# Kernel tuning notes

Measured on AMD Instinct MI355X. Metric: run time of the kernel, lower is better.

## Reference

```python
import math
import jax, jax.numpy as jnp
import numpy as np
from jax import lax

B, H, W = 8, 96, 96
FC, R, P, KS, TOPK = 768, 12, 16, 13, 24
SUP_TH, SUP_MIX, OPEN_K, DIL, NMS = 0.28, 0.8, 3, 3, 3

# prototype anchor metadata (buffers, deterministic)
ORI = jnp.asarray(np.linspace(0.0, math.pi, P + 1)[:-1], jnp.float32)
_lenL = np.array([0.4, 0.7, 1.0, 1.25], np.float32)
_widL = np.array([0.12, 0.18, 0.24, 0.3], np.float32)
LEN = jnp.asarray(_lenL[np.arange(P) % 4])
WID = jnp.asarray(_widL[(np.arange(P) // 4) % 4])
_ax = np.linspace(-1.0, 1.0, KS).astype(np.float32)
_gy, _gx = np.meshgrid(_ax, _ax, indexing='ij')
GX, GY = jnp.asarray(_gx), jnp.asarray(_gy)


def conv2d(x, w, b, pad=0):
    y = lax.conv_general_dilated(x, w, (1, 1), [(pad, pad), (pad, pad)],
                                 dimension_numbers=('NCHW', 'OIHW', 'NCHW'))
    return y + b[None, :, None, None]


def maxpool(x, k):
    p = k // 2
    return lax.reduce_window(x, -jnp.inf, lax.max, (1, 1, k, k), (1, 1, 1, 1),
                             [(0, 0), (0, 0), (p, p), (p, p)])


def avgpool3(x):
    s = lax.reduce_window(x, 0.0, lax.add, (1, 1, 3, 3), (1, 1, 1, 1),
                          [(0, 0), (0, 0), (1, 1), (1, 1)])
    return s / 9.0  # torch count_include_pad=True


def normalize_map(t):
    mn = t.min(axis=(-2, -1), keepdims=True)
    mx = t.max(axis=(-2, -1), keepdims=True)
    return (t - mn) / jnp.maximum(mx - mn, 1e-6)


def binary_open(m, k):
    er = 1.0 - maxpool(1.0 - m, k)
    return jnp.clip(maxpool(er, k), 0.0, 1.0)


def support_mask_fn(carrier_hp, density):
    cs = normalize_map(avgpool3(jnp.abs(carrier_hp)))
    ds = normalize_map(density)
    ev = SUP_MIX * cs + (1.0 - SUP_MIX) * ds
    m = (ev >= SUP_TH).astype(carrier_hp.dtype)
    m = binary_open(m, OPEN_K)
    m = maxpool(m, DIL)
    return jnp.clip(m, 0.0, 1.0)


def setup_inputs() -> dict:
    key = jax.random.key(0)
    ks = jax.random.split(key, 16)
    d = {
        'features': jax.random.normal(ks[0], (B, FC, H, W), jnp.float32),
        'carrier_hp': jax.random.normal(ks[1], (B, 1, H, W), jnp.float32),
        'density': jax.random.uniform(ks[2], (B, 1, H, W), jnp.float32),
        # feature_project: 1x1 conv FC->R, 3x3 conv R->R
        'w1': jax.random.normal(ks[3], (R, FC, 1, 1), jnp.float32) * (1.0 / math.sqrt(FC)),
        'b1': jnp.zeros((R,), jnp.float32),
        'w2': jax.random.normal(ks[4], (R, R, 3, 3), jnp.float32) * (1.0 / math.sqrt(R * 9)),
        'b2': jnp.zeros((R,), jnp.float32),
        # post_mix: 1x1 conv (R+4)->R, 1x1 conv R->FC
        'w3': jax.random.normal(ks[5], (R, R + 4, 1, 1), jnp.float32) * (1.0 / math.sqrt(R + 4)),
        'b3': jnp.zeros((R,), jnp.float32),
        'w4': jax.random.normal(ks[6], (FC, R, 1, 1), jnp.float32) * (1.0 / math.sqrt(R)),
        'b4': jnp.zeros((FC,), jnp.float32),
        'proto': jax.random.normal(ks[7], (P, R), jnp.float32) * 0.02,
    }
    return d


def reference(features, carrier_hp, density, w1, b1, w2, b2, w3, b3, w4, b4, proto):
    gelu = lambda x: jax.nn.gelu(x, approximate=False)
    # 1) feature projection
    proj = gelu(conv2d(gelu(conv2d(features, w1, b1, 0)), w2, b2, 1))  # [B,R,H,W]
    # 2) occupancy + support
    occ = normalize_map(jnp.abs(proj).mean(axis=1, keepdims=True))      # [B,1,H,W]
    sup = support_mask_fn(carrier_hp, density)                          # [B,1,H,W]
    # 3) NMS + top-k anchors
    scores = occ * sup
    local_max = maxpool(scores, NMS)
    peak = ((scores >= local_max) & (scores > 0.05)).astype(scores.dtype)
    flat = (scores * peak).reshape(B, -1)
    vals, idx = lax.top_k(flat, TOPK)                                   # [B,K]
    anchor_map = jnp.zeros_like(flat).at[jnp.arange(B)[:, None], idx].set(vals)
    anchor_map = anchor_map.reshape(B, 1, H, W)
    ys, xs = idx // W, idx % W
    # 4) per-anchor prototype selection
    proj_flat = proj.reshape(B, R, H * W)
    feat_at = jnp.take_along_axis(proj_flat, jnp.broadcast_to(idx[:, None, :], (B, R, TOPK)), axis=2)  # [B,R,K]
    logits = jnp.einsum('brk,pr->bkp', feat_at, proto)
    pidx = jnp.argmax(logits, axis=-1)                                  # [B,K]
    ori, ln, wd = ORI[pidx], LEN[pidx], WID[pidx]
    # 5) oriented Gaussian footprints [B,K,KS,KS]
    c = jnp.cos(ori)[..., None, None]
    s = jnp.sin(ori)[..., None, None]
    xr = c * GX + s * GY
    yr = -s * GX + c * GY
    foot = jnp.exp(-(xr / ln[..., None, None]) ** 2 - (yr / wd[..., None, None]) ** 2)
    foot = foot * vals[..., None, None]
    emb = proto[pidx]                                                   # [B,K,R]
    contrib = emb[:, :, :, None, None] * foot[:, :, None]               # [B,K,R,KS,KS]
    # 6) scatter-stamp onto canvas
    off = jnp.arange(KS) - KS // 2
    yy = ys[:, :, None, None] + off[None, None, :, None]                # [B,K,KS,KS]
    xx = xs[:, :, None, None] + off[None, None, None, :]
    valid = ((yy >= 0) & (yy < H) & (xx >= 0) & (xx < W)).astype(contrib.dtype)
    yyc = jnp.clip(yy, 0, H - 1)
    xxc = jnp.clip(xx, 0, W - 1)

    def stamp(ctr, y2, x2, v):
        c0 = jnp.zeros((R, H, W), ctr.dtype)
        return c0.at[:, y2, x2].add(jnp.transpose(ctr, (1, 0, 2, 3)) * v[None])

    canvas = jax.vmap(stamp)(contrib, yyc, xxc, valid)                  # [B,R,H,W]
    # 7) support-lock + post mix
    canvas = canvas * sup
    extras = jnp.concatenate([occ, sup, anchor_map, normalize_map(density)], axis=1)
    mixed = conv2d(gelu(conv2d(jnp.concatenate([canvas, extras], axis=1), w3, b3, 0)), w4, b4, 0)
    return mixed
```

## Files before the change

kernel.cpp:

```cpp
#include <hip/hip_runtime.h>
#include <math.h>

#define Bn 8
#define Hh 96
#define Ww 96
#define NPIX 9216
#define FCn 768
#define Rr 12
#define Pp 16
#define KSn 13
#define TOPKn 24
#define CAPc 1536
#define NSPLIT 8

__device__ __forceinline__ float gelu_f(float x) {
  return 0.5f * x * (1.0f + erff(x * 0.70710678118654752440f));
}

__global__ __launch_bounds__(256) void k_conv1_part(
    const float* __restrict__ feat, const float* __restrict__ w1,
    float* __restrict__ partial) {
  __shared__ float w1s[96 * 12];
  int s = blockIdx.x & 7;
  int pixblk = blockIdx.x >> 3;
  int c0 = s * 96;
  for (int i = threadIdx.x; i < 96 * 12; i += 256) {
    int c = i / 12, r = i % 12;
    w1s[i] = w1[r * FCn + c0 + c];
  }
  __syncthreads();
  int px0 = pixblk * 512 + threadIdx.x * 2;
  int b = px0 / NPIX, hw = px0 % NPIX;
  const float* fb = feat + (size_t)b * FCn * NPIX + (size_t)c0 * NPIX + hw;
  float acc0[12], acc1[12];
#pragma unroll
  for (int r = 0; r < 12; r++) { acc0[r] = 0.f; acc1[r] = 0.f; }
  for (int c = 0; c < 96; c += 4) {
    float2 f[4];
#pragma unroll
    for (int u = 0; u < 4; u++)
      f[u] = *(const float2*)(fb + (size_t)(c + u) * NPIX);
#pragma unroll
    for (int u = 0; u < 4; u++) {
#pragma unroll
      for (int r = 0; r < 12; r++) {
        float w = w1s[(c + u) * 12 + r];
        acc0[r] = fmaf(f[u].x, w, acc0[r]);
        acc1[r] = fmaf(f[u].y, w, acc1[r]);
      }
    }
  }
  float* outp = partial + (size_t)s * (Bn * Rr * NPIX) +
                (size_t)b * Rr * NPIX + hw;
#pragma unroll
  for (int r = 0; r < 12; r++)
    *(float2*)(outp + (size_t)r * NPIX) = make_float2(acc0[r], acc1[r]);
}

__global__ __launch_bounds__(256) void k_bias_gelu(
    const float* __restrict__ partial, const float* __restrict__ b1,
    float* __restrict__ t1, unsigned int* __restrict__ statsu) {
  int e4 = blockIdx.x * 256 + threadIdx.x;
  const int Q = (Bn * Rr * NPIX) / 4;
  const float4* pp = (const float4*)partial;
  float4 v = pp[e4];
#pragma unroll
  for (int s = 1; s < NSPLIT; s++) {
    float4 t = pp[e4 + s * Q];
    v.x += t.x; v.y += t.y; v.z += t.z; v.w += t.w;
  }
  int r = (e4 / (NPIX / 4)) % Rr;
  float bias = b1[r];
  float4 o;
  o.x = gelu_f(v.x + bias);
  o.y = gelu_f(v.y + bias);
  o.z = gelu_f(v.z + bias);
  o.w = gelu_f(v.w + bias);
  ((float4*)t1)[e4] = o;
  if (e4 < 24) {
    statsu[e4 * 2 + 0] = 0x7f800000u;
    statsu[e4 * 2 + 1] = 0u;
  }
}

__global__ __launch_bounds__(256) void k_conv2(
    const float* __restrict__ t1, const float* __restrict__ w2,
    const float* __restrict__ b2, const float* __restrict__ carrier,
    const float* __restrict__ density, float* __restrict__ proj,
    float* __restrict__ occ_raw, float* __restrict__ cs_raw,
    unsigned int* __restrict__ statsu, float* __restrict__ canvas,
    float* __restrict__ anchor) {
  __shared__ float w2s[Rr * Rr * 9];
  __shared__ float b2s[Rr];
  for (int i = threadIdx.x; i < Rr * Rr * 9; i += 256) w2s[i] = w2[i];
  if (threadIdx.x < Rr) b2s[threadIdx.x] = b2[threadIdx.x];
  int pix = blockIdx.x * 256 + threadIdx.x;
  {
    float4 z = make_float4(0.f, 0.f, 0.f, 0.f);
    float4* c4 = (float4*)canvas;
#pragma unroll
    for (int q = 0; q < 3; q++) c4[(size_t)q * (Bn * NPIX) + pix] = z;
    anchor[pix] = 0.f;
  }
  __syncthreads();
  int b = pix / NPIX, hw = pix % NPIX;
  int y = hw / Ww, x = hw % Ww;
  float acc[12];
#pragma unroll
  for (int r = 0; r < 12; r++) acc[r] = 0.f;
  const float* tb = t1 + (size_t)b * Rr * NPIX;
  for (int ri = 0; ri < Rr; ri++) {
    const float* tc = tb + (size_t)ri * NPIX;
#pragma unroll
    for (int ky = 0; ky < 3; ky++) {
      int yy = y + ky - 1;
      if (yy < 0 || yy >= Hh) continue;
#pragma unroll
      for (int kx = 0; kx < 3; kx++) {
        int xx = x + kx - 1;
        if (xx < 0 || xx >= Ww) continue;
        float v = tc[yy * Ww + xx];
#pragma unroll
        for (int ro = 0; ro < 12; ro++)
          acc[ro] = fmaf(v, w2s[((ro * Rr + ri) * 3 + ky) * 3 + kx], acc[ro]);
      }
    }
  }
  float asum = 0.f;
  float* pb = proj + (size_t)b * Rr * NPIX + hw;
#pragma unroll
  for (int ro = 0; ro < 12; ro++) {
    float g = gelu_f(acc[ro] + b2s[ro]);
    pb[(size_t)ro * NPIX] = g;
    asum += fabsf(g);
  }
  float occv = asum / 12.0f;
  occ_raw[pix] = occv;

  const float* cb = carrier + (size_t)b * NPIX;
  float s9 = 0.f;
  for (int dy = -1; dy <= 1; dy++) {
    int yy = y + dy;
    if (yy < 0 || yy >= Hh) continue;
    for (int dx = -1; dx <= 1; dx++) {
      int xx = x + dx;
      if (xx < 0 || xx >= Ww) continue;
      s9 += fabsf(cb[yy * Ww + xx]);
    }
  }
  float csv = s9 / 9.0f;
  cs_raw[pix] = csv;
  float dv = density[pix];

  float mn0 = occv, mx0 = occv, mn1 = csv, mx1 = csv, mn2 = dv, mx2 = dv;
#pragma unroll
  for (int off = 32; off > 0; off >>= 1) {
    mn0 = fminf(mn0, __shfl_xor(mn0, off));
    mx0 = fmaxf(mx0, __shfl_xor(mx0, off));
    mn1 = fminf(mn1, __shfl_xor(mn1, off));
    mx1 = fmaxf(mx1, __shfl_xor(mx1, off));
    mn2 = fminf(mn2, __shfl_xor(mn2, off));
    mx2 = fmaxf(mx2, __shfl_xor(mx2, off));
  }
  if ((threadIdx.x & 63) == 0) {
    atomicMin(&statsu[(0 * Bn + b) * 2 + 0], __float_as_uint(mn0));
    atomicMax(&statsu[(0 * Bn + b) * 2 + 1], __float_as_uint(mx0));
    atomicMin(&statsu[(1 * Bn + b) * 2 + 0], __float_as_uint(mn1));
    atomicMax(&statsu[(1 * Bn + b) * 2 + 1], __float_as_uint(mx1));
    atomicMin(&statsu[(2 * Bn + b) * 2 + 0], __float_as_uint(mn2));
    atomicMax(&statsu[(2 * Bn + b) * 2 + 1], __float_as_uint(mx2));
  }
}

__global__ __launch_bounds__(1024) void k_support_topk(
    const float* __restrict__ occ_raw, const float* __restrict__ cs_raw,
    const float* __restrict__ density, const float* __restrict__ stats,
    float* __restrict__ occ, float* __restrict__ ds, float* __restrict__ sup,
    float* __restrict__ vals, int* __restrict__ idxs,
    float* __restrict__ anchor) {
  __shared__ unsigned char mA[NPIX], mB[NPIX];
  __shared__ float flat[NPIX];
  __shared__ float cval[CAPc];
  __shared__ int cidx[CAPc];
  __shared__ int cnt;
  __shared__ float rv[16];
  __shared__ int ri[16], rs[16];
  int b = blockIdx.x;
  const int tid = threadIdx.x;
  const int lane = tid & 63, wid = tid >> 6;
  float omn = stats[(0 * Bn + b) * 2], omx = stats[(0 * Bn + b) * 2 + 1];
  float cmn = stats[(1 * Bn + b) * 2], cmx = stats[(1 * Bn + b) * 2 + 1];
  float dmn = stats[(2 * Bn + b) * 2], dmx = stats[(2 * Bn + b) * 2 + 1];
  float oiv = fmaxf(omx - omn, 1e-6f);
  float civ = fmaxf(cmx - cmn, 1e-6f);
  float div_ = fmaxf(dmx - dmn, 1e-6f);
  if (tid == 0) cnt = 0;
  float occ9[9];
#pragma unroll
  for (int i = 0; i < 9; i++) {
    int p = tid + i * 1024;
    float oc = (occ_raw[b * NPIX + p] - omn) / oiv;
    float cv = (cs_raw[b * NPIX + p] - cmn) / civ;
    float dv = (density[b * NPIX + p] - dmn) / div_;
    occ[b * NPIX + p] = oc;
    ds[b * NPIX + p] = dv;
    occ9[i] = oc;
    float ev = 0.8f * cv + 0.2f * dv;
    mA[p] = (ev >= 0.28f) ? 1 : 0;
  }
  __syncthreads();
#pragma unroll
  for (int i = 0; i < 9; i++) {
    int p = tid + i * 1024;
    int y = p / Ww, x = p % Ww;
    unsigned char m = 1;
    for (int dy = -1; dy <= 1; dy++) {
      int yy = y + dy;
      if (yy < 0 || yy >= Hh) continue;
      for (int dx = -1; dx <= 1; dx++) {
        int xx = x + dx;
        if (xx < 0 || xx >= Ww) continue;
        m = (unsigned char)(m & mA[yy * Ww + xx]);
      }
    }
    mB[p] = m;
  }
  __syncthreads();
#pragma unroll
  for (int i = 0; i < 9; i++) {
    int p = tid + i * 1024;
    int y = p / Ww, x = p % Ww;
    unsigned char m = 0;
    for (int dy = -1; dy <= 1; dy++) {
      int yy = y + dy;
      if (yy < 0 || yy >= Hh) continue;
      for (int dx = -1; dx <= 1; dx++) {
        int xx = x + dx;
        if (xx < 0 || xx >= Ww) continue;
        m = (unsigned char)(m | mB[yy * Ww + xx]);
      }
    }
    mA[p] = m;
  }
  __syncthreads();
#pragma unroll
  for (int i = 0; i < 9; i++) {
    int p = tid + i * 1024;
    int y = p / Ww, x = p % Ww;
    unsigned char m = 0;
    for (int dy = -1; dy <= 1; dy++) {
      int yy = y + dy;
      if (yy < 0 || yy >= Hh) continue;
      for (int dx = -1; dx <= 1; dx++) {
        int xx = x + dx;
        if (xx < 0 || xx >= Ww) continue;
        m = (unsigned char)(m | mA[yy * Ww + xx]);
      }
    }
    float sv = (float)m;
    sup[b * NPIX + p] = sv;
    flat[p] = occ9[i] * sv;
  }
  __syncthreads();
  float pk[9];
#pragma unroll
  for (int i = 0; i < 9; i++) {
    int p = tid + i * 1024;
    int y = p / Ww, x = p % Ww;
    float s = flat[p];
    float lm = -INFINITY;
    for (int dy = -1; dy <= 1; dy++) {
      int yy = y + dy;
      if (yy < 0 || yy >= Hh) continue;
      for (int dx = -1; dx <= 1; dx++) {
        int xx = x + dx;
        if (xx < 0 || xx >= Ww) continue;
        lm = fmaxf(lm, flat[yy * Ww + xx]);
      }
    }
    pk[i] = (s >= lm && s > 0.05f) ? s : 0.0f;
  }
  __syncthreads();
#pragma unroll
  for (int i = 0; i < 9; i++) {
    int p = tid + i * 1024;
    flat[p] = pk[i];
    if (pk[i] > 0.f) {
      int slot = atomicAdd(&cnt, 1);
      if (slot < CAPc) {
        cval[slot] = pk[i];
        cidx[slot] = p;
      }
    }
  }
  __syncthreads();
  const int C = cnt;
  if (C <= CAPc) {
    for (int k = 0; k < TOPKn; k++) {
      float bv = -INFINITY;
      int bi = 0x7fffffff, bs = -1;
      for (int j = tid; j < C; j += 1024) {
        float v = cval[j];
        int pi = cidx[j];
        if (v > bv || (v == bv && pi < bi)) {
          bv = v;
          bi = pi;
          bs = j;
        }
      }
      for (int off = 32; off > 0; off >>= 1) {
        float ov = __shfl_xor(bv, off);
        int oi = __shfl_xor(bi, off);
        int os = __shfl_xor(bs, off);
        if (ov > bv || (ov == bv && oi < bi)) {
          bv = ov;
          bi = oi;
          bs = os;
        }
      }
      if (lane == 0) {
        rv[wid] = bv;
        ri[wid] = bi;
        rs[wid] = bs;
      }
      __syncthreads();
      if (tid == 0) {
        float Bv = rv[0];
        int Bi = ri[0], Bs = rs[0];
        for (int w = 1; w < 16; w++) {
          if (rv[w] > Bv || (rv[w] == Bv && ri[w] < Bi)) {
            Bv = rv[w];
            Bi = ri[w];
            Bs = rs[w];
          }
        }
        if (Bv > 0.f) {
          vals[b * TOPKn + k] = Bv;
          idxs[b * TOPKn + k] = Bi;
          anchor[b * NPIX + Bi] = Bv;
          cval[Bs] = -INFINITY;
        } else {
          vals[b * TOPKn + k] = 0.f;
          idxs[b * TOPKn + k] = 0;
        }
      }
      __syncthreads();
    }
  } else {
    for (int k = 0; k < TOPKn; k++) {
      float bv = -INFINITY;
      int bi = 0x7fffffff;
      for (int p = tid; p < NPIX; p += 1024) {
        float v = flat[p];
        if (v > bv || (v == bv && p < bi)) {
          bv = v;
          bi = p;
        }
      }
      for (int off = 32; off > 0; off >>= 1) {
        float ov = __shfl_xor(bv, off);
        int oi = __shfl_xor(bi, off);
        if (ov > bv || (ov == bv && oi < bi)) {
          bv = ov;
          bi = oi;
        }
      }
      if (lane == 0) {
        rv[wid] = bv;
        ri[wid] = bi;
      }
      __syncthreads();
      if (tid == 0) {
        float Bv = rv[0];
        int Bi = ri[0];
        for (int w = 1; w < 16; w++) {
          if (rv[w] > Bv || (rv[w] == Bv && ri[w] < Bi)) {
            Bv = rv[w];
            Bi = ri[w];
          }
        }
        if (Bv > 0.f) {
          vals[b * TOPKn + k] = Bv;
          idxs[b * TOPKn + k] = Bi;
          anchor[b * NPIX + Bi] = Bv;
          flat[Bi] = -INFINITY;
        } else {
          vals[b * TOPKn + k] = 0.f;
          idxs[b * TOPKn + k] = 0;
        }
      }
      __syncthreads();
    }
  }
}

__global__ __launch_bounds__(192) void k_stamp(
    const float* __restrict__ proj, const float* __restrict__ proto,
    const float* __restrict__ vals, const int* __restrict__ idxs,
    float* __restrict__ canvas) {
  int b = blockIdx.x / TOPKn, k = blockIdx.x % TOPKn;
  __shared__ float embs[12];
  __shared__ float prm[5];
  __shared__ int ppos[2];
  if (threadIdx.x == 0) {
    int id = idxs[b * TOPKn + k];
    float v = vals[b * TOPKn + k];
    float ft[12];
    for (int r = 0; r < 12; r++)
      ft[r] = proj[(size_t)(b * Rr + r) * NPIX + id];
    float bestL = -INFINITY;
    int bp = 0;
    for (int p = 0; p < Pp; p++) {
      float L = 0.f;
      for (int r = 0; r < 12; r++) L = fmaf(ft[r], proto[p * Rr + r], L);
      if (L > bestL) {
        bestL = L;
        bp = p;
      }
    }
    const float lenL[4] = {0.4f, 0.7f, 1.0f, 1.25f};
    const float widL[4] = {0.12f, 0.18f, 0.24f, 0.3f};
    float ori = (float)((M_PI / 16.0) * (double)bp);
    prm[0] = cosf(ori);
    prm[1] = sinf(ori);
    prm[2] = lenL[bp & 3];
    prm[3] = widL[(bp >> 2) & 3];
    prm[4] = v;
    ppos[0] = id / Ww;
    ppos[1] = id % Ww;
    for (int r = 0; r < 12; r++) embs[r] = proto[bp * Rr + r];
  }
  __syncthreads();
  float v = prm[4];
  if (v <= 0.f) return;
  int t = threadIdx.x;
  if (t >= KSn * KSn) return;
  int i = t / KSn, j = t % KSn;
  float gx = (float)(-1.0 + (double)j * (1.0 / 6.0));
  float gy = (float)(-1.0 + (double)i * (1.0 / 6.0));
  float c = prm[0], s = prm[1];
  float xr = c * gx + s * gy;
  float yr = -s * gx + c * gy;
  float tx = xr / prm[2], ty = yr / prm[3];
  float foot = expf(-(tx * tx) - (ty * ty)) * v;
  int yy = ppos[0] + i - KSn / 2;
  int xx = ppos[1] + j - KSn / 2;
  if (yy < 0 || yy >= Hh || xx < 0 || xx >= Ww) return;
  float* cp = canvas + (size_t)b * Rr * NPIX + yy * Ww + xx;
#pragma unroll
  for (int r = 0; r < 12; r++) atomicAdd(cp + (size_t)r * NPIX, embs[r] * foot);
}

__global__ __launch_bounds__(256) void k_post1(
    const float* __restrict__ canvas, const float* __restrict__ sup,
    const float* __restrict__ occ, const float* __restrict__ anchor,
    const float* __restrict__ ds, const float* __restrict__ w3,
    const float* __restrict__ b3, float* __restrict__ h) {
  __shared__ float w3s[12 * 16], b3s[12];
  for (int i = threadIdx.x; i < 192; i += 256) w3s[i] = w3[i];
  if (threadIdx.x < 12) b3s[threadIdx.x] = b3[threadIdx.x];
  __syncthreads();
  int pix = blockIdx.x * 256 + threadIdx.x;
  int b = pix / NPIX, hw = pix % NPIX;
  float in16[16];
  float sv = sup[pix];
#pragma unroll
  for (int r = 0; r < 12; r++)
    in16[r] = canvas[(size_t)(b * Rr + r) * NPIX + hw] * sv;
  in16[12] = occ[pix];
  in16[13] = sv;
  in16[14] = anchor[pix];
  in16[15] = ds[pix];
  float* hb = h + (size_t)b * Rr * NPIX + hw;
#pragma unroll
  for (int ro = 0; ro < 12; ro++) {
    float acc = 0.f;
#pragma unroll
    for (int ci = 0; ci < 16; ci++)
      acc = fmaf(in16[ci], w3s[ro * 16 + ci], acc);
    hb[(size_t)ro * NPIX] = gelu_f(acc + b3s[ro]);
  }
}

__global__ __launch_bounds__(256) void k_post2(
    const float* __restrict__ h, const float* __restrict__ w4,
    const float* __restrict__ b4, float* __restrict__ out) {
  __shared__ float w4s[16 * 12], b4s[16];
  int bx = blockIdx.x;
  int hwblk = bx % 9;
  int g = (bx / 9) % 48;
  int b = bx / (9 * 48);
  int oc0 = g * 16;
  for (int i = threadIdx.x; i < 192; i += 256) w4s[i] = w4[oc0 * 12 + i];
  if (threadIdx.x < 16) b4s[threadIdx.x] = b4[oc0 + threadIdx.x];
  __syncthreads();
  int hw = hwblk * 1024 + threadIdx.x * 4;
  const float* hb = h + (size_t)b * Rr * NPIX + hw;
  float4 hreg[12];
#pragma unroll
  for (int r = 0; r < 12; r++)
    hreg[r] = *(const float4*)(hb + (size_t)r * NPIX);
  float* ob = out + (size_t)(b * FCn + oc0) * NPIX + hw;
#pragma unroll
  for (int j = 0; j < 16; j++) {
    float ax = 0.f, ay = 0.f, az = 0.f, aw = 0.f;
#pragma unroll
    for (int r = 0; r < 12; r++) {
      float w = w4s[j * 12 + r];
      ax = fmaf(hreg[r].x, w, ax);
      ay = fmaf(hreg[r].y, w, ay);
      az = fmaf(hreg[r].z, w, az);
      aw = fmaf(hreg[r].w, w, aw);
    }
    float bb = b4s[j];
    *(float4*)(ob + (size_t)j * NPIX) =
        make_float4(ax + bb, ay + bb, az + bb, aw + bb);
  }
}

extern "C" void kernel_launch(void* const* d_in, const int* in_sizes, int n_in,
                              void* d_out, int out_size, void* d_ws,
                              size_t ws_size, hipStream_t stream) {
  const float* features = (const float*)d_in[0];
  const float* carrier = (const float*)d_in[1];
  const float* density = (const float*)d_in[2];
  const float* w1 = (const float*)d_in[3];
  const float* b1 = (const float*)d_in[4];
  const float* w2 = (const float*)d_in[5];
  const float* b2 = (const float*)d_in[6];
  const float* w3 = (const float*)d_in[7];
  const float* b3 = (const float*)d_in[8];
  const float* w4 = (const float*)d_in[9];
  const float* b4 = (const float*)d_in[10];
  const float* proto = (const float*)d_in[11];
  float* out = (float*)d_out;
  float* ws = (float*)d_ws;

  const size_t NT = (size_t)Bn * Rr * NPIX;
  float* t1 = ws;
  float* partial = ws + NT;
  float* proj = partial;
  float* canvas = partial + NT;
  float* h = partial + 2 * NT;
  float* sm = ws + 9 * NT;
  float* occ_raw = sm;
  float* cs_raw = sm + (size_t)Bn * NPIX;
  float* occ = sm + 2 * (size_t)Bn * NPIX;
  float* ds = sm + 3 * (size_t)Bn * NPIX;
  float* sup = sm + 4 * (size_t)Bn * NPIX;
  float* anchor = sm + 5 * (size_t)Bn * NPIX;
  float* stats = sm + 6 * (size_t)Bn * NPIX;
  unsigned int* statsu = (unsigned int*)stats;
  float* vals = stats + 64;
  int* idxs = (int*)(vals + Bn * TOPKn);

  k_conv1_part<<<144 * NSPLIT, 256, 0, stream>>>(features, w1, partial);
  k_bias_gelu<<<(int)(NT / 4 / 256), 256, 0, stream>>>(partial, b1, t1, statsu);
  k_conv2<<<288, 256, 0, stream>>>(t1, w2, b2, carrier, density, proj, occ_raw,
                                   cs_raw, statsu, canvas, anchor);
  k_support_topk<<<Bn, 1024, 0, stream>>>(occ_raw, cs_raw, density, stats, occ,
                                          ds, sup, vals, idxs, anchor);
  k_stamp<<<Bn * TOPKn, 192, 0, stream>>>(proj, proto, vals, idxs, canvas);
  k_post1<<<288, 256, 0, stream>>>(canvas, sup, occ, anchor, ds, w3, b3, h);
  k_post2<<<Bn * 48 * 9, 256, 0, stream>>>(h, w4, b4, out);
}
```

Before: 577.6 us.

## Fold support-mask computation into conv1 launch and halve channel split

The support-mask pipeline (carrier avgpool, density normalization, morphological open and dilate) moves out of the serial 8-block topk kernel into 8 extra blocks of the conv1 launch, so it runs alongside the bandwidth-bound 1x1 conv. Each of those blocks computes its own carrier and density min/max with an intra-block reduction, so the cross-block atomics for those statistics are dropped. The conv1 channel split goes from 8 to 4, which halves the partial-sum traffic read by bias_gelu but gives each block twice as many channels and fewer blocks overall. The support blocks recompute the 3x3 carrier sums twice, and each is a single 256-thread block that may finish after the conv blocks, lengthening that launch.

```diff
diff --git a/kernel.cpp b/kernel.cpp
--- a/kernel.cpp
+++ b/kernel.cpp
@@ -11,50 +11,173 @@
 #define KSn 13
 #define TOPKn 24
 #define CAPc 1536
-#define NSPLIT 8
+#define NSPLIT 4
 
 __device__ __forceinline__ float gelu_f(float x) {
   return 0.5f * x * (1.0f + erff(x * 0.70710678118654752440f));
 }
 
-__global__ __launch_bounds__(256) void k_conv1_part(
+__global__ __launch_bounds__(256) void k_conv1_sup(
     const float* __restrict__ feat, const float* __restrict__ w1,
-    float* __restrict__ partial) {
-  __shared__ float w1s[96 * 12];
-  int s = blockIdx.x & 7;
-  int pixblk = blockIdx.x >> 3;
-  int c0 = s * 96;
-  for (int i = threadIdx.x; i < 96 * 12; i += 256) {
-    int c = i / 12, r = i % 12;
-    w1s[i] = w1[r * FCn + c0 + c];
-  }
-  __syncthreads();
-  int px0 = pixblk * 512 + threadIdx.x * 2;
-  int b = px0 / NPIX, hw = px0 % NPIX;
-  const float* fb = feat + (size_t)b * FCn * NPIX + (size_t)c0 * NPIX + hw;
-  float acc0[12], acc1[12];
-#pragma unroll
-  for (int r = 0; r < 12; r++) { acc0[r] = 0.f; acc1[r] = 0.f; }
-  for (int c = 0; c < 96; c += 4) {
-    float2 f[4];
-#pragma unroll
-    for (int u = 0; u < 4; u++)
-      f[u] = *(const float2*)(fb + (size_t)(c + u) * NPIX);
-#pragma unroll
-    for (int u = 0; u < 4; u++) {
-#pragma unroll
-      for (int r = 0; r < 12; r++) {
-        float w = w1s[(c + u) * 12 + r];
-        acc0[r] = fmaf(f[u].x, w, acc0[r]);
-        acc1[r] = fmaf(f[u].y, w, acc1[r]);
-      }
-    }
-  }
-  float* outp = partial + (size_t)s * (Bn * Rr * NPIX) +
-                (size_t)b * Rr * NPIX + hw;
-#pragma unroll
-  for (int r = 0; r < 12; r++)
-    *(float2*)(outp + (size_t)r * NPIX) = make_float2(acc0[r], acc1[r]);
+    float* __restrict__ partial, const float* __restrict__ carrier,
+    const float* __restrict__ density, float* __restrict__ sup,
+    float* __restrict__ ds) {
+  __shared__ __align__(16) unsigned char lds_raw[2 * NPIX];
+  __shared__ float red[16];
+  const int tid = threadIdx.x;
+  if (blockIdx.x >= 8) {
+    float* w1s = (float*)lds_raw;
+    int bx = blockIdx.x - 8;
+    int s = bx & 3;
+    int pixblk = bx >> 2;
+    int c0 = s * 192;
+    for (int i = tid; i < 192 * 12; i += 256) {
+      int c = i / 12, r = i % 12;
+      w1s[i] = w1[r * FCn + c0 + c];
+    }
+    __syncthreads();
+    int px0 = pixblk * 512 + tid * 2;
+    int b = px0 / NPIX, hw = px0 % NPIX;
+    const float* fb = feat + (size_t)b * FCn * NPIX + (size_t)c0 * NPIX + hw;
+    float acc0[12], acc1[12];
+#pragma unroll
+    for (int r = 0; r < 12; r++) { acc0[r] = 0.f; acc1[r] = 0.f; }
+    for (int c = 0; c < 192; c += 4) {
+      float2 f[4];
+#pragma unroll
+      for (int u = 0; u < 4; u++)
+        f[u] = *(const float2*)(fb + (size_t)(c + u) * NPIX);
+#pragma unroll
+      for (int u = 0; u < 4; u++) {
+#pragma unroll
+        for (int r = 0; r < 12; r++) {
+          float w = w1s[(c + u) * 12 + r];
+          acc0[r] = fmaf(f[u].x, w, acc0[r]);
+          acc1[r] = fmaf(f[u].y, w, acc1[r]);
+        }
+      }
+    }
+    float* outp = partial + (size_t)s * (Bn * Rr * NPIX) +
+                  (size_t)b * Rr * NPIX + hw;
+#pragma unroll
+    for (int r = 0; r < 12; r++)
+      *(float2*)(outp + (size_t)r * NPIX) = make_float2(acc0[r], acc1[r]);
+    return;
+  }
+  unsigned char* mA = lds_raw;
+  unsigned char* mB = lds_raw + NPIX;
+  int b = blockIdx.x;
+  const int lane = tid & 63, wid = tid >> 6;
+  const float* cb = carrier + (size_t)b * NPIX;
+  const float* db = density + (size_t)b * NPIX;
+  float cmn = INFINITY, cmx = -INFINITY, dmn = INFINITY, dmx = -INFINITY;
+  for (int i = 0; i < 36; i++) {
+    int p = tid + (i << 8);
+    int y = p / Ww, x = p % Ww;
+    float s9 = 0.f;
+    for (int dy = -1; dy <= 1; dy++) {
+      int yy = y + dy;
+      if (yy < 0 || yy >= Hh) continue;
+      for (int dx = -1; dx <= 1; dx++) {
+        int xx = x + dx;
+        if (xx < 0 || xx >= Ww) continue;
+        s9 += fabsf(cb[yy * Ww + xx]);
+      }
+    }
+    float cs = s9 / 9.0f;
+    cmn = fminf(cmn, cs);
+    cmx = fmaxf(cmx, cs);
+    float dv = db[p];
+    dmn = fminf(dmn, dv);
+    dmx = fmaxf(dmx, dv);
+  }
+#pragma unroll
+  for (int off = 32; off > 0; off >>= 1) {
+    cmn = fminf(cmn, __shfl_xor(cmn, off));
+    cmx = fmaxf(cmx, __shfl_xor(cmx, off));
+    dmn = fminf(dmn, __shfl_xor(dmn, off));
+    dmx = fmaxf(dmx, __shfl_xor(dmx, off));
+  }
+  if (lane == 0) {
+    red[wid * 4 + 0] = cmn;
+    red[wid * 4 + 1] = cmx;
+    red[wid * 4 + 2] = dmn;
+    red[wid * 4 + 3] = dmx;
+  }
+  __syncthreads();
+  cmn = fminf(fminf(red[0], red[4]), fminf(red[8], red[12]));
+  cmx = fmaxf(fmaxf(red[1], red[5]), fmaxf(red[9], red[13]));
+  dmn = fminf(fminf(red[2], red[6]), fminf(red[10], red[14]));
+  dmx = fmaxf(fmaxf(red[3], red[7]), fmaxf(red[11], red[15]));
+  float civ = fmaxf(cmx - cmn, 1e-6f);
+  float div_ = fmaxf(dmx - dmn, 1e-6f);
+  for (int i = 0; i < 36; i++) {
+    int p = tid + (i << 8);
+    int y = p / Ww, x = p % Ww;
+    float s9 = 0.f;
+    for (int dy = -1; dy <= 1; dy++) {
+      int yy = y + dy;
+      if (yy < 0 || yy >= Hh) continue;
+      for (int dx = -1; dx <= 1; dx++) {
+        int xx = x + dx;
+        if (xx < 0 || xx >= Ww) continue;
+        s9 += fabsf(cb[yy * Ww + xx]);
+      }
+    }
+    float cs = s9 / 9.0f;
+    float dn = (db[p] - dmn) / div_;
+    ds[(size_t)b * NPIX + p] = dn;
+    float ev = 0.8f * ((cs - cmn) / civ) + 0.2f * dn;
+    mA[p] = (ev >= 0.28f) ? 1 : 0;
+  }
+  __syncthreads();
+  for (int i = 0; i < 36; i++) {
+    int p = tid + (i << 8);
+    int y = p / Ww, x = p % Ww;
+    unsigned char m = 1;
+    for (int dy = -1; dy <= 1; dy++) {
+      int yy = y + dy;
+      if (yy < 0 || yy >= Hh) continue;
+      for (int dx = -1; dx <= 1; dx++) {
+        int xx = x + dx;
+        if (xx < 0 || xx >= Ww) continue;
+        m = (unsigned char)(m & mA[yy * Ww + xx]);
+      }
+    }
+    mB[p] = m;
+  }
+  __syncthreads();
+  for (int i = 0; i < 36; i++) {
+    int p = tid + (i << 8);
+    int y = p / Ww, x = p % Ww;
+    unsigned char m = 0;
+    for (int dy = -1; dy <= 1; dy++) {
+      int yy = y + dy;
+      if (yy < 0 || yy >= Hh) continue;
+      for (int dx = -1; dx <= 1; dx++) {
+        int xx = x + dx;
+        if (xx < 0 || xx >= Ww) continue;
+        m = (unsigned char)(m | mB[yy * Ww + xx]);
+      }
+    }
+    mA[p] = m;
+  }
+  __syncthreads();
+  for (int i = 0; i < 36; i++) {
+    int p = tid + (i << 8);
+    int y = p / Ww, x = p % Ww;
+    unsigned char m = 0;
+    for (int dy = -1; dy <= 1; dy++) {
+      int yy = y + dy;
+      if (yy < 0 || yy >= Hh) continue;
+      for (int dx = -1; dx <= 1; dx++) {
+        int xx = x + dx;
+        if (xx < 0 || xx >= Ww) continue;
+        m = (unsigned char)(m | mA[yy * Ww + xx]);
+      }
+    }
+    sup[(size_t)b * NPIX + p] = (float)m;
+  }
 }
 
 __global__ __launch_bounds__(256) void k_bias_gelu(
@@ -63,21 +186,16 @@
   int e4 = blockIdx.x * 256 + threadIdx.x;
   const int Q = (Bn * Rr * NPIX) / 4;
   const float4* pp = (const float4*)partial;
-  float4 v = pp[e4];
-#pragma unroll
-  for (int s = 1; s < NSPLIT; s++) {
-    float4 t = pp[e4 + s * Q];
-    v.x += t.x; v.y += t.y; v.z += t.z; v.w += t.w;
-  }
+  float4 a = pp[e4], b_ = pp[e4 + Q], c = pp[e4 + 2 * Q], d = pp[e4 + 3 * Q];
   int r = (e4 / (NPIX / 4)) % Rr;
   float bias = b1[r];
-  float4 o;
-  o.x = gelu_f(v.x + bias);
-  o.y = gelu_f(v.y + bias);
-  o.z = gelu_f(v.z + bias);
-  o.w = gelu_f(v.w + bias);
-  ((float4*)t1)[e4] = o;
-  if (e4 < 24) {
+  float4 v;
+  v.x = gelu_f(((a.x + b_.x) + c.x) + d.x + bias);
+  v.y = gelu_f(((a.y + b_.y) + c.y) + d.y + bias);
+  v.z = gelu_f(((a.z + b_.z) + c.z) + d.z + bias);
+  v.w = gelu_f(((a.w + b_.w) + c.w) + d.w + bias);
+  ((float4*)t1)[e4] = v;
+  if (e4 < Bn) {
     statsu[e4 * 2 + 0] = 0x7f800000u;
     statsu[e4 * 2 + 1] = 0u;
   }
@@ -85,11 +203,9 @@
 
 __global__ __launch_bounds__(256) void k_conv2(
     const float* __restrict__ t1, const float* __restrict__ w2,
-    const float* __restrict__ b2, const float* __restrict__ carrier,
-    const float* __restrict__ density, float* __restrict__ proj,
-    float* __restrict__ occ_raw, float* __restrict__ cs_raw,
-    unsigned int* __restrict__ statsu, float* __restrict__ canvas,
-    float* __restrict__ anchor) {
+    const float* __restrict__ b2, float* __restrict__ proj,
+    float* __restrict__ occ_raw, unsigned int* __restrict__ statsu,
+    float* __restrict__ canvas, float* __restrict__ anchor) {
   __shared__ float w2s[Rr * Rr * 9];
   __shared__ float b2s[Rr];
   for (int i = threadIdx.x; i < Rr * Rr * 9; i += 256) w2s[i] = w2[i];
@@ -137,48 +253,23 @@
   float occv = asum / 12.0f;
   occ_raw[pix] = occv;
 
-  const float* cb = carrier + (size_t)b * NPIX;
-  float s9 = 0.f;
-  for (int dy = -1; dy <= 1; dy++) {
-    int yy = y + dy;
-    if (yy < 0 || yy >= Hh) continue;
-    for (int dx = -1; dx <= 1; dx++) {
-      int xx = x + dx;
-      if (xx < 0 || xx >= Ww) continue;
-      s9 += fabsf(cb[yy * Ww + xx]);
-    }
-  }
-  float csv = s9 / 9.0f;
-  cs_raw[pix] = csv;
-  float dv = density[pix];
-
-  float mn0 = occv, mx0 = occv, mn1 = csv, mx1 = csv, mn2 = dv, mx2 = dv;
+  float mn0 = occv, mx0 = occv;
 #pragma unroll
   for (int off = 32; off > 0; off >>= 1) {
     mn0 = fminf(mn0, __shfl_xor(mn0, off));
     mx0 = fmaxf(mx0, __shfl_xor(mx0, off));
-    mn1 = fminf(mn1, __shfl_xor(mn1, off));
-    mx1 = fmaxf(mx1, __shfl_xor(mx1, off));
-    mn2 = fminf(mn2, __shfl_xor(mn2, off));
-    mx2 = fmaxf(mx2, __shfl_xor(mx2, off));
   }
   if ((threadIdx.x & 63) == 0) {
-    atomicMin(&statsu[(0 * Bn + b) * 2 + 0], __float_as_uint(mn0));
-    atomicMax(&statsu[(0 * Bn + b) * 2 + 1], __float_as_uint(mx0));
-    atomicMin(&statsu[(1 * Bn + b) * 2 + 0], __float_as_uint(mn1));
-    atomicMax(&statsu[(1 * Bn + b) * 2 + 1], __float_as_uint(mx1));
-    atomicMin(&statsu[(2 * Bn + b) * 2 + 0], __float_as_uint(mn2));
-    atomicMax(&statsu[(2 * Bn + b) * 2 + 1], __float_as_uint(mx2));
-  }
-}
-
-__global__ __launch_bounds__(1024) void k_support_topk(
-    const float* __restrict__ occ_raw, const float* __restrict__ cs_raw,
-    const float* __restrict__ density, const float* __restrict__ stats,
-    float* __restrict__ occ, float* __restrict__ ds, float* __restrict__ sup,
+    atomicMin(&statsu[b * 2 + 0], __float_as_uint(mn0));
+    atomicMax(&statsu[b * 2 + 1], __float_as_uint(mx0));
+  }
+}
+
+__global__ __launch_bounds__(1024) void k_topk(
+    const float* __restrict__ occ_raw, const float* __restrict__ stats,
+    const float* __restrict__ sup_g, float* __restrict__ occ,
     float* __restrict__ vals, int* __restrict__ idxs,
     float* __restrict__ anchor) {
-  __shared__ unsigned char mA[NPIX], mB[NPIX];
   __shared__ float flat[NPIX];
   __shared__ float cval[CAPc];
   __shared__ int cidx[CAPc];
@@ -188,78 +279,15 @@
   int b = blockIdx.x;
   const int tid = threadIdx.x;
   const int lane = tid & 63, wid = tid >> 6;
-  float omn = stats[(0 * Bn + b) * 2], omx = stats[(0 * Bn + b) * 2 + 1];
-  float cmn = stats[(1 * Bn + b) * 2], cmx = stats[(1 * Bn + b) * 2 + 1];
-  float dmn = stats[(2 * Bn + b) * 2], dmx = stats[(2 * Bn + b) * 2 + 1];
+  float omn = stats[b * 2 + 0], omx = stats[b * 2 + 1];
   float oiv = fmaxf(omx - omn, 1e-6f);
-  float civ = fmaxf(cmx - cmn, 1e-6f);
-  float div_ = fmaxf(dmx - dmn, 1e-6f);
   if (tid == 0) cnt = 0;
-  float occ9[9];
 #pragma unroll
   for (int i = 0; i < 9; i++) {
     int p = tid + i * 1024;
-    float oc = (occ_raw[b * NPIX + p] - omn) / oiv;
-    float cv = (cs_raw[b * NPIX + p] - cmn) / civ;
-    float dv = (density[b * NPIX + p] - dmn) / div_;
-    occ[b * NPIX + p] = oc;
-    ds[b * NPIX + p] = dv;
-    occ9[i] = oc;
-    float ev = 0.8f * cv + 0.2f * dv;
-    mA[p] = (ev >= 0.28f) ? 1 : 0;
-  }
-  __syncthreads();
-#pragma unroll
-  for (int i = 0; i < 9; i++) {
-    int p = tid + i * 1024;
-    int y = p / Ww, x = p % Ww;
-    unsigned char m = 1;
-    for (int dy = -1; dy <= 1; dy++) {
-      int yy = y + dy;
-      if (yy < 0 || yy >= Hh) continue;
-      for (int dx = -1; dx <= 1; dx++) {
-        int xx = x + dx;
-        if (xx < 0 || xx >= Ww) continue;
-        m = (unsigned char)(m & mA[yy * Ww + xx]);
-      }
-    }
-    mB[p] = m;
-  }
-  __syncthreads();
-#pragma unroll
-  for (int i = 0; i < 9; i++) {
-    int p = tid + i * 1024;
-    int y = p / Ww, x = p % Ww;
-    unsigned char m = 0;
-    for (int dy = -1; dy <= 1; dy++) {
-      int yy = y + dy;
-      if (yy < 0 || yy >= Hh) continue;
-      for (int dx = -1; dx <= 1; dx++) {
-        int xx = x + dx;
-        if (xx < 0 || xx >= Ww) continue;
-        m = (unsigned char)(m | mB[yy * Ww + xx]);
-      }
-    }
-    mA[p] = m;
-  }
-  __syncthreads();
-#pragma unroll
-  for (int i = 0; i < 9; i++) {
-    int p = tid + i * 1024;
-    int y = p / Ww, x = p % Ww;
-    unsigned char m = 0;
-    for (int dy = -1; dy <= 1; dy++) {
-      int yy = y + dy;
-      if (yy < 0 || yy >= Hh) continue;
-      for (int dx = -1; dx <= 1; dx++) {
-        int xx = x + dx;
-        if (xx < 0 || xx >= Ww) continue;
-        m = (unsigned char)(m | mA[yy * Ww + xx]);
-      }
-    }
-    float sv = (float)m;
-    sup[b * NPIX + p] = sv;
-    flat[p] = occ9[i] * sv;
+    float oc = (occ_raw[(size_t)b * NPIX + p] - omn) / oiv;
+    occ[(size_t)b * NPIX + p] = oc;
+    flat[p] = oc * sup_g[(size_t)b * NPIX + p];
   }
   __syncthreads();
   float pk[9];
@@ -337,7 +365,7 @@
         if (Bv > 0.f) {
           vals[b * TOPKn + k] = Bv;
           idxs[b * TOPKn + k] = Bi;
-          anchor[b * NPIX + Bi] = Bv;
+          anchor[(size_t)b * NPIX + Bi] = Bv;
           cval[Bs] = -INFINITY;
         } else {
           vals[b * TOPKn + k] = 0.f;
@@ -382,7 +410,7 @@
         if (Bv > 0.f) {
           vals[b * TOPKn + k] = Bv;
           idxs[b * TOPKn + k] = Bi;
-          anchor[b * NPIX + Bi] = Bv;
+          anchor[(size_t)b * NPIX + Bi] = Bv;
           flat[Bi] = -INFINITY;
         } else {
           vals[b * TOPKn + k] = 0.f;
@@ -542,24 +570,23 @@
   float* proj = partial;
   float* canvas = partial + NT;
   float* h = partial + 2 * NT;
-  float* sm = ws + 9 * NT;
+  float* sm = ws + 5 * NT;
   float* occ_raw = sm;
-  float* cs_raw = sm + (size_t)Bn * NPIX;
-  float* occ = sm + 2 * (size_t)Bn * NPIX;
-  float* ds = sm + 3 * (size_t)Bn * NPIX;
-  float* sup = sm + 4 * (size_t)Bn * NPIX;
-  float* anchor = sm + 5 * (size_t)Bn * NPIX;
-  float* stats = sm + 6 * (size_t)Bn * NPIX;
+  float* occ = sm + (size_t)Bn * NPIX;
+  float* ds = sm + 2 * (size_t)Bn * NPIX;
+  float* sup = sm + 3 * (size_t)Bn * NPIX;
+  float* anchor = sm + 4 * (size_t)Bn * NPIX;
+  float* stats = sm + 5 * (size_t)Bn * NPIX;
   unsigned int* statsu = (unsigned int*)stats;
   float* vals = stats + 64;
   int* idxs = (int*)(vals + Bn * TOPKn);
 
-  k_conv1_part<<<144 * NSPLIT, 256, 0, stream>>>(features, w1, partial);
+  k_conv1_sup<<<8 + 144 * NSPLIT, 256, 0, stream>>>(features, w1, partial,
+                                                    carrier, density, sup, ds);
   k_bias_gelu<<<(int)(NT / 4 / 256), 256, 0, stream>>>(partial, b1, t1, statsu);
-  k_conv2<<<288, 256, 0, stream>>>(t1, w2, b2, carrier, density, proj, occ_raw,
-                                   cs_raw, statsu, canvas, anchor);
-  k_support_topk<<<Bn, 1024, 0, stream>>>(occ_raw, cs_raw, density, stats, occ,
-                                          ds, sup, vals, idxs, anchor);
+  k_conv2<<<288, 256, 0, stream>>>(t1, w2, b2, proj, occ_raw, statsu, canvas,
+                                   anchor);
+  k_topk<<<Bn, 1024, 0, stream>>>(occ_raw, stats, sup, occ, vals, idxs, anchor);
   k_stamp<<<Bn * TOPKn, 192, 0, stream>>>(proj, proto, vals, idxs, canvas);
   k_post1<<<288, 256, 0, stream>>>(canvas, sup, occ, anchor, ds, w3, b3, h);
   k_post2<<<Bn * 48 * 9, 256, 0, stream>>>(h, w4, b4, out);
```

After: 712.8 us. 23.4% more time.

## Halve conv1 channel split and fuse stamping into support/top-k kernel

Applied to the files above, without the earlier changes.

Reduces the channel split of the 1x1 conv from 8 to 4, so each block handles 192 channels, which halves the partial-sum buffer traffic and the reduction work in bias+GELU. It also folds the stamp kernel into the per-batch support/top-k kernel, removing one launch and the round-trip of vals/idxs through global memory. In exchange, conv1 launches half as many blocks with longer loops, and the stamping now runs on only 8 blocks instead of 192, so less parallelism is available for the atomics.

```diff
diff --git a/kernel.cpp b/kernel.cpp
--- a/kernel.cpp
+++ b/kernel.cpp
@@ -11,7 +11,7 @@
 #define KSn 13
 #define TOPKn 24
 #define CAPc 1536
-#define NSPLIT 8
+#define NSPLIT 4
 
 __device__ __forceinline__ float gelu_f(float x) {
   return 0.5f * x * (1.0f + erff(x * 0.70710678118654752440f));
@@ -20,11 +20,11 @@
 __global__ __launch_bounds__(256) void k_conv1_part(
     const float* __restrict__ feat, const float* __restrict__ w1,
     float* __restrict__ partial) {
-  __shared__ float w1s[96 * 12];
-  int s = blockIdx.x & 7;
-  int pixblk = blockIdx.x >> 3;
-  int c0 = s * 96;
-  for (int i = threadIdx.x; i < 96 * 12; i += 256) {
+  __shared__ float w1s[192 * 12];
+  int s = blockIdx.x & 3;
+  int pixblk = blockIdx.x >> 2;
+  int c0 = s * 192;
+  for (int i = threadIdx.x; i < 192 * 12; i += 256) {
     int c = i / 12, r = i % 12;
     w1s[i] = w1[r * FCn + c0 + c];
   }
@@ -35,7 +35,7 @@
   float acc0[12], acc1[12];
 #pragma unroll
   for (int r = 0; r < 12; r++) { acc0[r] = 0.f; acc1[r] = 0.f; }
-  for (int c = 0; c < 96; c += 4) {
+  for (int c = 0; c < 192; c += 4) {
     float2 f[4];
 #pragma unroll
     for (int u = 0; u < 4; u++)
@@ -63,20 +63,15 @@
   int e4 = blockIdx.x * 256 + threadIdx.x;
   const int Q = (Bn * Rr * NPIX) / 4;
   const float4* pp = (const float4*)partial;
-  float4 v = pp[e4];
-#pragma unroll
-  for (int s = 1; s < NSPLIT; s++) {
-    float4 t = pp[e4 + s * Q];
-    v.x += t.x; v.y += t.y; v.z += t.z; v.w += t.w;
-  }
+  float4 a = pp[e4], b_ = pp[e4 + Q], c = pp[e4 + 2 * Q], d = pp[e4 + 3 * Q];
   int r = (e4 / (NPIX / 4)) % Rr;
   float bias = b1[r];
-  float4 o;
-  o.x = gelu_f(v.x + bias);
-  o.y = gelu_f(v.y + bias);
-  o.z = gelu_f(v.z + bias);
-  o.w = gelu_f(v.w + bias);
-  ((float4*)t1)[e4] = o;
+  float4 v;
+  v.x = gelu_f(((a.x + b_.x) + c.x) + d.x + bias);
+  v.y = gelu_f(((a.y + b_.y) + c.y) + d.y + bias);
+  v.z = gelu_f(((a.z + b_.z) + c.z) + d.z + bias);
+  v.w = gelu_f(((a.w + b_.w) + c.w) + d.w + bias);
+  ((float4*)t1)[e4] = v;
   if (e4 < 24) {
     statsu[e4 * 2 + 0] = 0x7f800000u;
     statsu[e4 * 2 + 1] = 0u;
@@ -172,12 +167,13 @@
   }
 }
 
-__global__ __launch_bounds__(1024) void k_support_topk(
+__global__ __launch_bounds__(1024) void k_support_topk_stamp(
     const float* __restrict__ occ_raw, const float* __restrict__ cs_raw,
     const float* __restrict__ density, const float* __restrict__ stats,
     float* __restrict__ occ, float* __restrict__ ds, float* __restrict__ sup,
     float* __restrict__ vals, int* __restrict__ idxs,
-    float* __restrict__ anchor) {
+    float* __restrict__ anchor, const float* __restrict__ proj,
+    const float* __restrict__ proto, float* __restrict__ canvas) {
   __shared__ unsigned char mA[NPIX], mB[NPIX];
   __shared__ float flat[NPIX];
   __shared__ float cval[CAPc];
@@ -185,6 +181,11 @@
   __shared__ int cnt;
   __shared__ float rv[16];
   __shared__ int ri[16], rs[16];
+  __shared__ float selv[TOPKn];
+  __shared__ int seli[TOPKn];
+  __shared__ float sprm[TOPKn][5];
+  __shared__ float semb[TOPKn][12];
+  __shared__ int spos[TOPKn][2];
   int b = blockIdx.x;
   const int tid = threadIdx.x;
   const int lane = tid & 63, wid = tid >> 6;
@@ -337,11 +338,15 @@
         if (Bv > 0.f) {
           vals[b * TOPKn + k] = Bv;
           idxs[b * TOPKn + k] = Bi;
-          anchor[b * NPIX + Bi] = Bv;
+          anchor[(size_t)b * NPIX + Bi] = Bv;
           cval[Bs] = -INFINITY;
+          selv[k] = Bv;
+          seli[k] = Bi;
         } else {
           vals[b * TOPKn + k] = 0.f;
           idxs[b * TOPKn + k] = 0;
+          selv[k] = 0.f;
+          seli[k] = 0;
         }
       }
       __syncthreads();
@@ -382,73 +387,77 @@
         if (Bv > 0.f) {
           vals[b * TOPKn + k] = Bv;
           idxs[b * TOPKn + k] = Bi;
-          anchor[b * NPIX + Bi] = Bv;
+          anchor[(size_t)b * NPIX + Bi] = Bv;
           flat[Bi] = -INFINITY;
+          selv[k] = Bv;
+          seli[k] = Bi;
         } else {
           vals[b * TOPKn + k] = 0.f;
           idxs[b * TOPKn + k] = 0;
+          selv[k] = 0.f;
+          seli[k] = 0;
         }
       }
       __syncthreads();
     }
   }
-}
-
-__global__ __launch_bounds__(192) void k_stamp(
-    const float* __restrict__ proj, const float* __restrict__ proto,
-    const float* __restrict__ vals, const int* __restrict__ idxs,
-    float* __restrict__ canvas) {
-  int b = blockIdx.x / TOPKn, k = blockIdx.x % TOPKn;
-  __shared__ float embs[12];
-  __shared__ float prm[5];
-  __shared__ int ppos[2];
-  if (threadIdx.x == 0) {
-    int id = idxs[b * TOPKn + k];
-    float v = vals[b * TOPKn + k];
-    float ft[12];
+  if (tid < TOPKn) {
+    int k = tid;
+    float v = selv[k];
+    int id = seli[k];
+    float c = 0.f, s = 0.f, ln = 1.f, wd = 1.f;
+    if (v > 0.f) {
+      float ft[12];
+      for (int r = 0; r < 12; r++)
+        ft[r] = proj[(size_t)(b * Rr + r) * NPIX + id];
+      float bestL = -INFINITY;
+      int bp = 0;
+      for (int p = 0; p < Pp; p++) {
+        float L = 0.f;
+        for (int r = 0; r < 12; r++) L = fmaf(ft[r], proto[p * Rr + r], L);
+        if (L > bestL) {
+          bestL = L;
+          bp = p;
+        }
+      }
+      const float lenL[4] = {0.4f, 0.7f, 1.0f, 1.25f};
+      const float widL[4] = {0.12f, 0.18f, 0.24f, 0.3f};
+      float ori = (float)((M_PI / 16.0) * (double)bp);
+      c = cosf(ori);
+      s = sinf(ori);
+      ln = lenL[bp & 3];
+      wd = widL[(bp >> 2) & 3];
+      for (int r = 0; r < 12; r++) semb[k][r] = proto[bp * Rr + r];
+    }
+    sprm[k][0] = c;
+    sprm[k][1] = s;
+    sprm[k][2] = ln;
+    sprm[k][3] = wd;
+    sprm[k][4] = v;
+    spos[k][0] = id / Ww;
+    spos[k][1] = id % Ww;
+  }
+  __syncthreads();
+  for (int t = tid; t < TOPKn * KSn * KSn; t += 1024) {
+    int k = t / (KSn * KSn), cell = t % (KSn * KSn);
+    float v = sprm[k][4];
+    if (v <= 0.f) continue;
+    int i = cell / KSn, j = cell % KSn;
+    float gx = (float)(-1.0 + (double)j * (1.0 / 6.0));
+    float gy = (float)(-1.0 + (double)i * (1.0 / 6.0));
+    float c = sprm[k][0], s = sprm[k][1];
+    float xr = c * gx + s * gy;
+    float yr = -s * gx + c * gy;
+    float tx = xr / sprm[k][2], ty = yr / sprm[k][3];
+    float foot = expf(-(tx * tx) - (ty * ty)) * v;
+    int yy = spos[k][0] + i - KSn / 2;
+    int xx = spos[k][1] + j - KSn / 2;
+    if (yy < 0 || yy >= Hh || xx < 0 || xx >= Ww) continue;
+    float* cp = canvas + (size_t)b * Rr * NPIX + yy * Ww + xx;
+#pragma unroll
     for (int r = 0; r < 12; r++)
-      ft[r] = proj[(size_t)(b * Rr + r) * NPIX + id];
-    float bestL = -INFINITY;
-    int bp = 0;
-    for (int p = 0; p < Pp; p++) {
-      float L = 0.f;
-      for (int r = 0; r < 12; r++) L = fmaf(ft[r], proto[p * Rr + r], L);
-      if (L > bestL) {
-        bestL = L;
-        bp = p;
-      }
-    }
-    const float lenL[4] = {0.4f, 0.7f, 1.0f, 1.25f};
-    const float widL[4] = {0.12f, 0.18f, 0.24f, 0.3f};
-    float ori = (float)((M_PI / 16.0) * (double)bp);
-    prm[0] = cosf(ori);
-    prm[1] = sinf(ori);
-    prm[2] = lenL[bp & 3];
-    prm[3] = widL[(bp >> 2) & 3];
-    prm[4] = v;
-    ppos[0] = id / Ww;
-    ppos[1] = id % Ww;
-    for (int r = 0; r < 12; r++) embs[r] = proto[bp * Rr + r];
-  }
-  __syncthreads();
-  float v = prm[4];
-  if (v <= 0.f) return;
-  int t = threadIdx.x;
-  if (t >= KSn * KSn) return;
-  int i = t / KSn, j = t % KSn;
-  float gx = (float)(-1.0 + (double)j * (1.0 / 6.0));
-  float gy = (float)(-1.0 + (double)i * (1.0 / 6.0));
-  float c = prm[0], s = prm[1];
-  float xr = c * gx + s * gy;
-  float yr = -s * gx + c * gy;
-  float tx = xr / prm[2], ty = yr / prm[3];
-  float foot = expf(-(tx * tx) - (ty * ty)) * v;
-  int yy = ppos[0] + i - KSn / 2;
-  int xx = ppos[1] + j - KSn / 2;
-  if (yy < 0 || yy >= Hh || xx < 0 || xx >= Ww) return;
-  float* cp = canvas + (size_t)b * Rr * NPIX + yy * Ww + xx;
-#pragma unroll
-  for (int r = 0; r < 12; r++) atomicAdd(cp + (size_t)r * NPIX, embs[r] * foot);
+      atomicAdd(cp + (size_t)r * NPIX, semb[k][r] * foot);
+  }
 }
 
 __global__ __launch_bounds__(256) void k_post1(
@@ -542,7 +551,7 @@
   float* proj = partial;
   float* canvas = partial + NT;
   float* h = partial + 2 * NT;
-  float* sm = ws + 9 * NT;
+  float* sm = ws + 5 * NT;
   float* occ_raw = sm;
   float* cs_raw = sm + (size_t)Bn * NPIX;
   float* occ = sm + 2 * (size_t)Bn * NPIX;
@@ -558,9 +567,9 @@
   k_bias_gelu<<<(int)(NT / 4 / 256), 256, 0, stream>>>(partial, b1, t1, statsu);
   k_conv2<<<288, 256, 0, stream>>>(t1, w2, b2, carrier, density, proj, occ_raw,
                                    cs_raw, statsu, canvas, anchor);
-  k_support_topk<<<Bn, 1024, 0, stream>>>(occ_raw, cs_raw, density, stats, occ,
-                                          ds, sup, vals, idxs, anchor);
-  k_stamp<<<Bn * TOPKn, 192, 0, stream>>>(proj, proto, vals, idxs, canvas);
+  k_support_topk_stamp<<<Bn, 1024, 0, stream>>>(occ_raw, cs_raw, density, stats,
+                                                occ, ds, sup, vals, idxs,
+                                                anchor, proj, proto, canvas);
   k_post1<<<288, 256, 0, stream>>>(canvas, sup, occ, anchor, ds, w3, b3, h);
   k_post2<<<Bn * 48 * 9, 256, 0, stream>>>(h, w4, b4, out);
 }
```

Result: no change. 580.7 us (+0.5%).
